# Kernel optimization log

Measured on AMD Instinct MI355X. Metric: run time of the kernel, lower is better.

## Reference

```python
import jax, jax.numpy as jnp
import numpy as np

B, N, H = 8, 128, 512   # batch, num_sent (n == m required by the 'all' branch), hidden_size
D = 2 * H               # bi-LSTM output dim
SCALE = 0.05


def setup_inputs() -> dict:
    key = jax.random.key(0)
    ks = jax.random.split(key, 24)
    p = lambda k, shape: (jax.random.normal(k, shape, dtype=jnp.float32) * SCALE)
    return {
        "x0_enc": jax.random.normal(ks[0], (B, N, D), dtype=jnp.float32),
        "x1_enc": jax.random.normal(ks[1], (B, N, D), dtype=jnp.float32),
        # concat_attention
        "Wc1": p(ks[2], (D, H)), "Wc2": p(ks[3], (D, H)), "vc": p(ks[4], (H,)),
        # bilinear_attention
        "Wb": p(ks[5], (D, D)),
        # dot_attention x2 (separate params)
        "Wd1": p(ks[6], (D, H)), "vd1": p(ks[7], (H,)),
        "Wd2": p(ks[8], (D, H)), "vd2": p(ks[9], (H,)),
        # minus_attention (Ws/vs are unused in forward)
        "Wm": p(ks[10], (D, H)), "vm": p(ks[11], (H,)),
        # aggregation_layer
        "Wq": p(ks[12], (D, H)), "vq": p(ks[13], (H,)),
        "Wp1": p(ks[14], (2 * D, H)), "Wp2": p(ks[15], (D, H)), "vp": p(ks[16], (H,)),
        "Wpred": p(ks[17], (2 * D, 2)), "bpred": jnp.zeros((2,), dtype=jnp.float32),
    }


def _dot_att(x, y, Wd, vd):
    # sjt[b,m,n] = vd . tanh(Wd(x[b,n] * y[b,m]))  -- pairwise elementwise product + MLP
    z = jnp.tanh(jnp.einsum("bnd,bmd,dh->bmnh", x, y, Wd))  # [B,m,n,H]
    s = jnp.einsum("bmnh,h->bmn", z, vd)
    a = jax.nn.softmax(s, axis=2)
    return jnp.einsum("bmn,bnd->bmd", a, x)


def _minus_att(x, y, Wm, vm):
    # Wm is linear, so Wm(x_n - y_m) = (x@Wm)_n - (y@Wm)_m
    a, b = x @ Wm, y @ Wm                                    # [B,n,H], [B,m,H]
    z = jnp.tanh(a[:, None, :, :] - b[:, :, None, :])        # [B,m,n,H]
    s = jnp.einsum("bmnh,h->bmn", z, vm)
    att = jax.nn.softmax(s, axis=2)
    return jnp.einsum("bmn,bnd->bmd", att, x)


def _concat_att(x, y, Wc1, Wc2, vc):
    a, b = x @ Wc1, y @ Wc2                                  # [B,n,H], [B,m,H]
    z = jnp.tanh(a[:, None, :, :] + b[:, :, None, :])        # [B,m,n,H]
    s = jnp.einsum("bmnh,h->bmn", z, vc)
    att = jax.nn.softmax(s, axis=2)
    return jnp.einsum("bmn,bnd->bmd", att, x)


def _bilinear_att(x, y, Wb):
    s = jnp.einsum("bmd,bnd->bmn", y, x @ Wb)
    att = jax.nn.softmax(s, axis=2)
    return jnp.einsum("bmn,bnd->bmd", att, x)


def reference(x0_enc, x1_enc, Wc1, Wc2, vc, Wb, Wd1, vd1, Wd2, vd2, Wm, vm,
              Wq, vq, Wp1, Wp2, vp, Wpred, bpred):
    x0, x1 = x0_enc, x1_enc
    # attention_fx('all')
    qtc = _concat_att(x0, x1, Wc1, Wc2, vc)
    qtb = _bilinear_att(x0, x1, Wb)
    qts = _dot_att(x0, x1, Wd1, vd1)
    qtd = _dot_att(x1, x0, Wd2, vd2)
    qtm = _minus_att(x0, x1, Wm, vm)
    agg_res = jnp.max(jnp.stack([x1, qts, qtc, qtd, qtb, qtm], axis=0), axis=0)  # [B,m,2H]
    # MultiAtt: dropout is identity in eval
    agg_rep = jnp.concatenate([x1, agg_res], axis=2)                             # [B,m,4H]
    # aggregation_layer
    sj = jnp.einsum("bnh,h->bn", jnp.tanh(x0 @ Wq), vq)
    rq = jnp.einsum("bn,bnd->bd", jax.nn.softmax(sj, axis=1), x0)                # [B,2H]
    t = agg_rep @ Wp1 + (rq @ Wp2)[:, None, :]                                   # [B,m,H]
    sp = jax.nn.softmax(jnp.einsum("bmh,h->bm", t, vp), axis=1)
    rp = jnp.einsum("bm,bmd->bd", sp, agg_rep)                                   # [B,4H]
    out = jax.nn.relu(rp @ Wpred + bpred)                                        # [B,2]
    return out
```

## Files before the change

### kernel.cpp

```cpp
#include <hip/hip_runtime.h>
#include <hip/hip_bf16.h>

static constexpr int Bc = 8, Nc = 128, Dc = 1024, Hc = 512;
static constexpr int BM = Bc * Nc;

typedef _Float16 half8 __attribute__((ext_vector_type(8)));
typedef __fp16 fp16x2 __attribute__((ext_vector_type(2)));
typedef float floatx4 __attribute__((ext_vector_type(4)));

__device__ __forceinline__ float fast_tanh(float x) {
  x = fminf(fmaxf(x, -15.f), 15.f);
  float e = __expf(2.f * x);
  return (e - 1.f) / (e + 1.f);
}

__device__ __forceinline__ unsigned pkh2(float a, float b) {
  fp16x2 h = __builtin_amdgcn_cvt_pkrtz(a, b);
  return __builtin_bit_cast(unsigned, h);
}

__device__ __forceinline__ ushort f2h(float f) {
  _Float16 h = (_Float16)f;
  return __builtin_bit_cast(ushort, h);
}

__device__ __forceinline__ float block_sum256(float v, float* buf4) {
  #pragma unroll
  for (int o = 32; o; o >>= 1) v += __shfl_down(v, o, 64);
  const int w = threadIdx.x >> 6, lane = threadIdx.x & 63;
  if (lane == 0) buf4[w] = v;
  __syncthreads();
  return buf4[0] + buf4[1] + buf4[2] + buf4[3];
}

__global__ __launch_bounds__(256) void cvt_both(const float* __restrict__ x0,
                                                const float* __restrict__ x1,
                                                ushort* __restrict__ o0,
                                                ushort* __restrict__ o1) {
  int bi = blockIdx.x;
  const float* src = (bi < 512) ? x0 : x1;
  ushort* dst = (bi < 512) ? o0 : o1;
  int off = (bi & 511);
  int i = (off * 256 + threadIdx.x) * 8;
  float4 a = *reinterpret_cast<const float4*>(&src[i]);
  float4 b = *reinterpret_cast<const float4*>(&src[i + 4]);
  uint4 o;
  o.x = pkh2(a.x, a.y); o.y = pkh2(a.z, a.w);
  o.z = pkh2(b.x, b.y); o.w = pkh2(b.z, b.w);
  *reinterpret_cast<uint4*>(&dst[i]) = o;
}

struct TJobs {
  const float* src[7];
  ushort* dst[7];
  int J[7];
};
__global__ __launch_bounds__(256) void conv_transpose_multi(TJobs jobs) {
  const int job = blockIdx.z;
  const int J = jobs.J[job];
  const int h0 = blockIdx.y * 64;
  if (h0 >= J) return;
  const float* W = jobs.src[job];
  ushort* WT = jobs.dst[job];
  __shared__ float tile[64][65];
  const int d0 = blockIdx.x * 64;
  const int tid = threadIdx.x;
  #pragma unroll
  for (int i = 0; i < 16; i++) {
    int idx = tid + i * 256;
    int dd = idx >> 6, hh = idx & 63;
    tile[dd][hh] = W[(size_t)(d0 + dd) * J + h0 + hh];
  }
  __syncthreads();
  #pragma unroll
  for (int i = 0; i < 16; i++) {
    int idx = tid + i * 256;
    int hh = idx >> 6, dd = idx & 63;
    WT[(size_t)(h0 + hh) * Dc + d0 + dd] = f2h(tile[dd][hh]);
  }
}

__global__ __launch_bounds__(256) void gemm_bt(const ushort* __restrict__ A,
                                               const ushort* __restrict__ BT,
                                               float* __restrict__ Cf,
                                               ushort* __restrict__ Ch,
                                               int K, int ldc,
                                               size_t sA, size_t sB, size_t sC) {
  const int bz = blockIdx.z;
  A  += (size_t)bz * sA;
  BT += (size_t)bz * sB;
  const int m0 = blockIdx.y * 64, n0 = blockIdx.x * 64;
  __shared__ __align__(16) ushort Asl[64][40];
  __shared__ __align__(16) ushort Bsl[64][40];
  const int tid = threadIdx.x, wave = tid >> 6, lane = tid & 63;
  const int quad = lane >> 4, l15 = lane & 15;
  const int wr = (wave & 1) * 32, wc = (wave >> 1) * 32;
  const int rSt = tid >> 2, kSt8 = (tid & 3) * 8;
  floatx4 acc[2][2];
  #pragma unroll
  for (int i = 0; i < 2; i++)
    #pragma unroll
    for (int j = 0; j < 2; j++) acc[i][j] = (floatx4){0.f, 0.f, 0.f, 0.f};
  uint4 pa = *reinterpret_cast<const uint4*>(&A[(size_t)(m0 + rSt) * K + kSt8]);
  uint4 pb = *reinterpret_cast<const uint4*>(&BT[(size_t)(n0 + rSt) * K + kSt8]);
  for (int k0 = 0; k0 < K; k0 += 32) {
    *reinterpret_cast<uint4*>(&Asl[rSt][kSt8]) = pa;
    *reinterpret_cast<uint4*>(&Bsl[rSt][kSt8]) = pb;
    __syncthreads();
    if (k0 + 32 < K) {
      pa = *reinterpret_cast<const uint4*>(&A[(size_t)(m0 + rSt) * K + k0 + 32 + kSt8]);
      pb = *reinterpret_cast<const uint4*>(&BT[(size_t)(n0 + rSt) * K + k0 + 32 + kSt8]);
    }
    half8 af[2], bb[2];
    #pragma unroll
    for (int i = 0; i < 2; i++)
      af[i] = *reinterpret_cast<const half8*>(&Asl[wr + i * 16 + l15][quad * 8]);
    #pragma unroll
    for (int j = 0; j < 2; j++)
      bb[j] = *reinterpret_cast<const half8*>(&Bsl[wc + j * 16 + l15][quad * 8]);
    #pragma unroll
    for (int i = 0; i < 2; i++)
      #pragma unroll
      for (int j = 0; j < 2; j++)
        acc[i][j] = __builtin_amdgcn_mfma_f32_16x16x32_f16(af[i], bb[j], acc[i][j], 0, 0, 0);
    __syncthreads();
  }
  if (Ch) {
    #pragma unroll
    for (int i = 0; i < 2; i++)
      #pragma unroll
      for (int j = 0; j < 2; j++)
        #pragma unroll
        for (int r = 0; r < 4; r++) {
          int row = m0 + wr + i * 16 + quad * 4 + r;
          int col = n0 + wc + j * 16 + l15;
          Ch[(size_t)bz * sC + (size_t)row * ldc + col] = f2h(acc[i][j][r]);
        }
  } else {
    #pragma unroll
    for (int i = 0; i < 2; i++)
      #pragma unroll
      for (int j = 0; j < 2; j++)
        #pragma unroll
        for (int r = 0; r < 4; r++) {
          int row = m0 + wr + i * 16 + quad * 4 + r;
          int col = n0 + wc + j * 16 + l15;
          Cf[(size_t)bz * sC + (size_t)row * ldc + col] = acc[i][j][r];
        }
  }
}

__global__ __launch_bounds__(512, 2) void dot_scores_mfma7(const ushort* __restrict__ X0h,
                                                           const ushort* __restrict__ X1h,
                                                           const ushort* __restrict__ WdT1,
                                                           const ushort* __restrict__ WdT2,
                                                           const float* __restrict__ vd1,
                                                           const float* __restrict__ vd2,
                                                           float* __restrict__ Sd) {
  const int which = blockIdx.z;
  const ushort* Xh = which ? X1h : X0h;
  const ushort* Yh = which ? X0h : X1h;
  const ushort* WdT = which ? WdT2 : WdT1;
  const float* v = which ? vd2 : vd1;
  float* S = Sd + (size_t)which * (BM * Nc);

  const int mp = blockIdx.y;
  const int b = mp >> 6;
  const int hBase = blockIdx.x * 256;
  const int tid = threadIdx.x;
  const int wave = tid >> 6, lane = tid & 63;
  const int quad = lane >> 4, l15 = lane & 15;
  const int mg = wave >> 2, wn = (wave >> 1) & 1, wh = wave & 1;

  __shared__ __align__(16) char smraw[36864];
  ushort* As = (ushort*)smraw;
  ushort* Bs = (ushort*)(smraw + 16384);
  ushort* ylh = (ushort*)(smraw + 32768);
  float (*red)[33] = (float(*)[33])smraw;

  {
    const uint* Y0 = (const uint*)(Yh + (size_t)(mp * 2) * Dc);
    uint* dst = (uint*)ylh;
    dst[tid] = Y0[tid];
    dst[tid + 512] = Y0[tid + 512];
  }

  floatx4 acc[4][8];
  #pragma unroll
  for (int i = 0; i < 4; i++)
    #pragma unroll
    for (int j = 0; j < 8; j++) acc[i][j] = (floatx4){0.f, 0.f, 0.f, 0.f};

  const ushort* Xb = Xh + (size_t)b * Nc * Dc;
  const int nA = tid >> 2;
  const int ch8 = (tid & 3) * 8;

  half8 xv;
  uint4 bv0, bv1;
  auto loads = [&](int s) {
    xv = *reinterpret_cast<const half8*>(Xb + (size_t)nA * Dc + s * 32 + ch8);
    const ushort* wp = WdT + (size_t)(hBase + nA) * Dc + s * 32 + ch8;
    bv0 = *reinterpret_cast<const uint4*>(wp);
    bv1 = *reinterpret_cast<const uint4*>(wp + 128 * Dc);
  };
  auto stage = [&](int s) {
    half8 y0 = *reinterpret_cast<const half8*>(ylh + s * 32 + ch8);
    half8 y1 = *reinterpret_cast<const half8*>(ylh + 1024 + s * 32 + ch8);
    *reinterpret_cast<half8*>(As + (size_t)nA * 32 + ch8) = xv * y0;
    *reinterpret_cast<half8*>(As + 4096 + (size_t)nA * 32 + ch8) = xv * y1;
    *reinterpret_cast<uint4*>(Bs + (size_t)nA * 32 + ch8) = bv0;
    *reinterpret_cast<uint4*>(Bs + 4096 + (size_t)nA * 32 + ch8) = bv1;
  };
  auto mfma_step = [&]() {
    half8 af[4], bfr[8];
    #pragma unroll
    for (int i = 0; i < 4; i++)
      af[i] = *reinterpret_cast<const half8*>(As + mg * 4096 + (wn * 64 + i * 16 + l15) * 32 + quad * 8);
    #pragma unroll
    for (int j = 0; j < 8; j++)
      bfr[j] = *reinterpret_cast<const half8*>(Bs + (wh * 128 + j * 16 + l15) * 32 + quad * 8);
    #pragma unroll
    for (int i = 0; i < 4; i++)
      #pragma unroll
      for (int j = 0; j < 8; j++)
        acc[i][j] = __builtin_amdgcn_mfma_f32_16x16x32_f16(af[i], bfr[j], acc[i][j], 0, 0, 0);
  };

  loads(0);
  __syncthreads();
  #pragma unroll 1
  for (int s = 0; s < 32; s++) {
    stage(s);
    if (s + 1 < 32) loads(s + 1);
    __syncthreads();
    mfma_step();
    __syncthreads();
  }

  float vv[8];
  #pragma unroll
  for (int j = 0; j < 8; j++) vv[j] = v[hBase + wh * 128 + j * 16 + l15];
  #pragma unroll
  for (int i = 0; i < 4; i++)
    #pragma unroll
    for (int r = 0; r < 4; r++) {
      float p = 0.f;
      #pragma unroll
      for (int j = 0; j < 8; j++) p = fmaf(vv[j], fast_tanh(acc[i][j][r]), p);
      red[mg * 128 + wn * 64 + i * 16 + quad * 4 + r][wh * 16 + l15] = p;
    }
  __syncthreads();
  if (tid < 256) {
    float s = 0.f;
    #pragma unroll
    for (int c = 0; c < 32; c++) s += red[tid][c];
    atomicAdd(&S[(size_t)mp * 256 + tid], s);
  }
}

__global__ __launch_bounds__(256) void addtanh_tiled2(const float* __restrict__ C1,
                                                      const float* __restrict__ C2,
                                                      const float* __restrict__ vc,
                                                      const float* __restrict__ vm,
                                                      float* __restrict__ Sc,
                                                      float* __restrict__ Sm) {
  const int nt = blockIdx.x, mt = blockIdx.y;
  const int which = blockIdx.z >> 3, b = blockIdx.z & 7;
  const float* Arow = C1 + which * 512;
  const float* Brow = C2 + which * 512;
  const float* v = which ? vm : vc;
  const float sign = which ? -1.f : 1.f;
  float* S = which ? Sm : Sc;
  __shared__ __align__(16) float at[16][516];
  __shared__ __align__(16) float bt2[16][516];
  __shared__ __align__(16) float vl[512];
  const int tid = threadIdx.x;
  #pragma unroll
  for (int p = 0; p < 8; p++) {
    int idx = p * 256 + tid;
    int r = idx >> 7, c4 = (idx & 127) * 4;
    *reinterpret_cast<float4*>(&at[r][c4]) =
        *reinterpret_cast<const float4*>(&Arow[(size_t)(b * Nc + nt * 16 + r) * 1024 + c4]);
    *reinterpret_cast<float4*>(&bt2[r][c4]) =
        *reinterpret_cast<const float4*>(&Brow[(size_t)(b * Nc + mt * 16 + r) * 1024 + c4]);
  }
  if (tid < 128)
    *reinterpret_cast<float4*>(&vl[tid * 4]) = *reinterpret_cast<const float4*>(&v[tid * 4]);
  __syncthreads();
  const int m = tid >> 4, n = tid & 15;
  float acc = 0.f;
  #pragma unroll 4
  for (int c = 0; c < 512; c += 4) {
    float4 av = *reinterpret_cast<const float4*>(&at[n][c]);
    float4 bv = *reinterpret_cast<const float4*>(&bt2[m][c]);
    float4 vv = *reinterpret_cast<const float4*>(&vl[c]);
    acc = fmaf(vv.x, fast_tanh(fmaf(sign, bv.x, av.x)), acc);
    acc = fmaf(vv.y, fast_tanh(fmaf(sign, bv.y, av.y)), acc);
    acc = fmaf(vv.z, fast_tanh(fmaf(sign, bv.z, av.z)), acc);
    acc = fmaf(vv.w, fast_tanh(fmaf(sign, bv.w, av.w)), acc);
  }
  S[(size_t)(b * Nc + mt * 16 + m) * Nc + nt * 16 + n] = acc;
}

__global__ __launch_bounds__(128) void softmax128(float* __restrict__ S) {
  const int row = blockIdx.x;
  const int tid = threadIdx.x;
  float x = S[(size_t)row * 128 + tid];
  __shared__ float mbuf[2], sbuf[2];
  float mx = x;
  #pragma unroll
  for (int o = 32; o; o >>= 1) mx = fmaxf(mx, __shfl_down(mx, o, 64));
  if ((tid & 63) == 0) mbuf[tid >> 6] = mx;
  __syncthreads();
  mx = fmaxf(mbuf[0], mbuf[1]);
  float e = __expf(x - mx);
  float sm = e;
  #pragma unroll
  for (int o = 32; o; o >>= 1) sm += __shfl_down(sm, o, 64);
  if ((tid & 63) == 0) sbuf[tid >> 6] = sm;
  __syncthreads();
  sm = sbuf[0] + sbuf[1];
  S[(size_t)row * 128 + tid] = e / sm;
}

#define FMA4(acc, s, v)                  \
  acc.x = fmaf(s, v.x, acc.x);           \
  acc.y = fmaf(s, v.y, acc.y);           \
  acc.z = fmaf(s, v.z, acc.z);           \
  acc.w = fmaf(s, v.w, acc.w)

__global__ __launch_bounds__(256) void agg_max(const float* __restrict__ x0,
                                               const float* __restrict__ x1,
                                               const float* __restrict__ Sc,
                                               const float* __restrict__ Sb,
                                               const float* __restrict__ Sd1,
                                               const float* __restrict__ Sd2,
                                               const float* __restrict__ Sm,
                                               const float* __restrict__ u,
                                               float* __restrict__ agg,
                                               float* __restrict__ score) {
  const int bm = blockIdx.x;
  const int b = bm >> 7;
  const int tid = threadIdx.x;
  __shared__ float w[5][128];
  if (tid < 128) {
    w[0][tid] = Sc[(size_t)bm * Nc + tid];
    w[1][tid] = Sb[(size_t)bm * Nc + tid];
    w[2][tid] = Sd1[(size_t)bm * Nc + tid];
    w[3][tid] = Sd2[(size_t)bm * Nc + tid];
    w[4][tid] = Sm[(size_t)bm * Nc + tid];
  }
  __syncthreads();
  const int d0 = tid * 4;
  float4 qc = {0, 0, 0, 0}, qb = {0, 0, 0, 0}, qs = {0, 0, 0, 0};
  float4 qd = {0, 0, 0, 0}, qm = {0, 0, 0, 0};
  const float* X0b = x0 + (size_t)b * Nc * Dc;
  const float* X1b = x1 + (size_t)b * Nc * Dc;
  for (int n = 0; n < Nc; n++) {
    float4 xv = *reinterpret_cast<const float4*>(&X0b[(size_t)n * Dc + d0]);
    float4 yv = *reinterpret_cast<const float4*>(&X1b[(size_t)n * Dc + d0]);
    float wc = w[0][n], wb = w[1][n], ws = w[2][n], wd = w[3][n], wm = w[4][n];
    FMA4(qc, wc, xv);
    FMA4(qb, wb, xv);
    FMA4(qs, ws, xv);
    FMA4(qd, wd, yv);
    FMA4(qm, wm, xv);
  }
  float4 x1v = *reinterpret_cast<const float4*>(&x1[(size_t)bm * Dc + d0]);
  float4 r;
  r.x = fmaxf(x1v.x, fmaxf(fmaxf(qs.x, qc.x), fmaxf(fmaxf(qd.x, qb.x), qm.x)));
  r.y = fmaxf(x1v.y, fmaxf(fmaxf(qs.y, qc.y), fmaxf(fmaxf(qd.y, qb.y), qm.y)));
  r.z = fmaxf(x1v.z, fmaxf(fmaxf(qs.z, qc.z), fmaxf(fmaxf(qd.z, qb.z), qm.z)));
  r.w = fmaxf(x1v.w, fmaxf(fmaxf(qs.w, qc.w), fmaxf(fmaxf(qd.w, qb.w), qm.w)));
  *reinterpret_cast<float4*>(&agg[(size_t)bm * Dc + d0]) = r;
  float4 u1 = *reinterpret_cast<const float4*>(&u[d0]);
  float4 u2 = *reinterpret_cast<const float4*>(&u[Dc + d0]);
  float p = x1v.x * u1.x + x1v.y * u1.y + x1v.z * u1.z + x1v.w * u1.w +
            r.x * u2.x + r.y * u2.y + r.z * u2.z + r.w * u2.w;
  __shared__ float buf4[4];
  p = block_sum256(p, buf4);
  if (tid == 0) score[bm] = p;
}

__global__ __launch_bounds__(64) void compute_u(const float* __restrict__ Wp1,
                                                const float* __restrict__ vp,
                                                float* __restrict__ u) {
  const int d2 = blockIdx.x;
  const int tid = threadIdx.x;
  float p = 0.f;
  #pragma unroll
  for (int h = tid; h < Hc; h += 64) p = fmaf(Wp1[(size_t)d2 * Hc + h], vp[h], p);
  #pragma unroll
  for (int o = 32; o; o >>= 1) p += __shfl_down(p, o, 64);
  if (tid == 0) u[d2] = p;
}

__global__ __launch_bounds__(256) void final_out(const float* __restrict__ x1,
                                                 const float* __restrict__ agg,
                                                 const float* __restrict__ score,
                                                 const float* __restrict__ Wpred,
                                                 const float* __restrict__ bpred,
                                                 float* __restrict__ out) {
  const int b = blockIdx.x;
  const int tid = threadIdx.x;
  __shared__ float spL[128];
  __shared__ float mbuf[2], sbuf[2];
  if (tid < 128) {
    float x = score[b * Nc + tid];
    float mx = x;
    #pragma unroll
    for (int o = 32; o; o >>= 1) mx = fmaxf(mx, __shfl_down(mx, o, 64));
    if ((tid & 63) == 0) mbuf[tid >> 6] = mx;
  }
  __syncthreads();
  if (tid < 128) {
    float x = score[b * Nc + tid];
    float mx = fmaxf(mbuf[0], mbuf[1]);
    float e = __expf(x - mx);
    float sm = e;
    #pragma unroll
    for (int o = 32; o; o >>= 1) sm += __shfl_down(sm, o, 64);
    if ((tid & 63) == 0) sbuf[tid >> 6] = sm;
    spL[tid] = e;
  }
  __syncthreads();
  const float inv = 1.f / (sbuf[0] + sbuf[1]);
  const int d2 = tid * 8;
  float w0[8], w1[8];
  #pragma unroll
  for (int i = 0; i < 8; i++) {
    w0[i] = Wpred[(size_t)(d2 + i) * 2 + 0];
    w1[i] = Wpred[(size_t)(d2 + i) * 2 + 1];
  }
  const float* src = (d2 < Dc) ? (x1 + (size_t)b * Nc * Dc + d2)
                               : (agg + (size_t)b * Nc * Dc + (d2 - Dc));
  float p0 = 0.f, p1 = 0.f;
  for (int m = 0; m < Nc; m++) {
    float s = spL[m] * inv;
    const float* r = src + (size_t)m * Dc;
    #pragma unroll
    for (int i = 0; i < 8; i++) {
      float sc = s * r[i];
      p0 = fmaf(sc, w0[i], p0);
      p1 = fmaf(sc, w1[i], p1);
    }
  }
  #pragma unroll
  for (int o = 32; o; o >>= 1) {
    p0 += __shfl_down(p0, o, 64);
    p1 += __shfl_down(p1, o, 64);
  }
  __shared__ float r0[4], r1[4];
  const int w = tid >> 6, lane = tid & 63;
  if (lane == 0) { r0[w] = p0; r1[w] = p1; }
  __syncthreads();
  if (tid == 0) {
    float q0 = r0[0] + r0[1] + r0[2] + r0[3] + bpred[0];
    float q1 = r1[0] + r1[1] + r1[2] + r1[3] + bpred[1];
    out[b * 2 + 0] = fmaxf(q0, 0.f);
    out[b * 2 + 1] = fmaxf(q1, 0.f);
  }
}

extern "C" void kernel_launch(void* const* d_in, const int* in_sizes, int n_in,
                              void* d_out, int out_size, void* d_ws, size_t ws_size,
                              hipStream_t stream) {
  const float* x0    = (const float*)d_in[0];
  const float* x1    = (const float*)d_in[1];
  const float* Wc1   = (const float*)d_in[2];
  const float* Wc2   = (const float*)d_in[3];
  const float* vc    = (const float*)d_in[4];
  const float* Wb    = (const float*)d_in[5];
  const float* Wd1   = (const float*)d_in[6];
  const float* vd1   = (const float*)d_in[7];
  const float* Wd2   = (const float*)d_in[8];
  const float* vd2   = (const float*)d_in[9];
  const float* Wm    = (const float*)d_in[10];
  const float* vm    = (const float*)d_in[11];
  const float* Wp1   = (const float*)d_in[14];
  const float* vp    = (const float*)d_in[16];
  const float* Wpred = (const float*)d_in[17];
  const float* bpred = (const float*)d_in[18];
  float* out = (float*)d_out;

  float* ws = (float*)d_ws;
  float* C1     = ws;
  float* C2     = C1 + 1048576;
  float* sc     = C2 + 1048576;
  float* sb     = sc + 131072;
  float* sd1    = sb + 131072;
  float* sd2    = sd1 + 131072;
  float* smv    = sd2 + 131072;
  float* u      = smv + 131072;
  float* score2 = u + 2048;
  ushort* x0h   = (ushort*)(score2 + 1024);
  ushort* x1h   = x0h + 1048576;
  ushort* W1T   = x1h + 1048576;
  ushort* W2T   = W1T + 1048576;
  ushort* WbT   = W2T + 1048576;
  ushort* xWbh  = WbT + 1048576;
  ushort* wdT1  = xWbh + 1048576;
  ushort* wdT2  = wdT1 + 524288;
  float* agg    = C1;

  cvt_both<<<1024, 256, 0, stream>>>(x0, x1, x0h, x1h);
  TJobs tj;
  tj.src[0] = Wd1; tj.dst[0] = wdT1;            tj.J[0] = Hc;
  tj.src[1] = Wd2; tj.dst[1] = wdT2;            tj.J[1] = Hc;
  tj.src[2] = Wc1; tj.dst[2] = W1T;             tj.J[2] = Hc;
  tj.src[3] = Wm;  tj.dst[3] = W1T + 512 * Dc;  tj.J[3] = Hc;
  tj.src[4] = Wc2; tj.dst[4] = W2T;             tj.J[4] = Hc;
  tj.src[5] = Wm;  tj.dst[5] = W2T + 512 * Dc;  tj.J[5] = Hc;
  tj.src[6] = Wb;  tj.dst[6] = WbT;             tj.J[6] = Dc;
  conv_transpose_multi<<<dim3(16, 16, 7), 256, 0, stream>>>(tj);
  compute_u<<<2 * Dc, 64, 0, stream>>>(Wp1, vp, u);

  gemm_bt<<<dim3(16, 16, 1), 256, 0, stream>>>(x0h, W1T, C1, nullptr, Dc, 1024, 0, 0, 0);
  gemm_bt<<<dim3(16, 16, 1), 256, 0, stream>>>(x1h, W2T, C2, nullptr, Dc, 1024, 0, 0, 0);
  gemm_bt<<<dim3(16, 16, 1), 256, 0, stream>>>(x0h, WbT, nullptr, xWbh, Dc, 1024, 0, 0, 0);
  gemm_bt<<<dim3(2, 2, 8), 256, 0, stream>>>(x1h, xWbh, sb, nullptr, Dc, 128,
                                             131072, 131072, 16384);

  addtanh_tiled2<<<dim3(8, 8, 16), 256, 0, stream>>>(C1, C2, vc, vm, sc, smv);

  (void)hipMemsetAsync(sd1, 0, 2 * 131072 * sizeof(float), stream);
  dot_scores_mfma7<<<dim3(2, BM / 2, 2), 512, 0, stream>>>(x0h, x1h, wdT1, wdT2, vd1, vd2, sd1);

  softmax128<<<5 * BM, 128, 0, stream>>>(sc);

  agg_max<<<BM, 256, 0, stream>>>(x0, x1, sc, sb, sd1, sd2, smv, u, agg, score2);

  final_out<<<Bc, 256, 0, stream>>>(x1, agg, score2, Wpred, bpred, out);
}
```

Before: 612.5 us.

## Double-buffer LDS in dot-score kernel and apply y-scaling at fragment load

```diff
diff --git a/kernel.cpp b/kernel.cpp
--- a/kernel.cpp
+++ b/kernel.cpp
@@ -150,7 +150,7 @@
   }
 }
 
-__global__ __launch_bounds__(512, 2) void dot_scores_mfma7(const ushort* __restrict__ X0h,
+__global__ __launch_bounds__(512, 2) void dot_scores_mfma8(const ushort* __restrict__ X0h,
                                                            const ushort* __restrict__ X1h,
                                                            const ushort* __restrict__ WdT1,
                                                            const ushort* __restrict__ WdT2,
@@ -172,10 +172,12 @@
   const int quad = lane >> 4, l15 = lane & 15;
   const int mg = wave >> 2, wn = (wave >> 1) & 1, wh = wave & 1;
 
-  __shared__ __align__(16) char smraw[36864];
-  ushort* As = (ushort*)smraw;
-  ushort* Bs = (ushort*)(smraw + 16384);
-  ushort* ylh = (ushort*)(smraw + 32768);
+  __shared__ __align__(16) char smraw[53248];
+  ushort* As0 = (ushort*)smraw;
+  ushort* As1 = (ushort*)(smraw + 8192);
+  ushort* Bs0 = (ushort*)(smraw + 16384);
+  ushort* Bs1 = (ushort*)(smraw + 32768);
+  ushort* ylh = (ushort*)(smraw + 49152);
   float (*red)[33] = (float(*)[33])smraw;
 
   {
@@ -203,22 +205,22 @@
     bv0 = *reinterpret_cast<const uint4*>(wp);
     bv1 = *reinterpret_cast<const uint4*>(wp + 128 * Dc);
   };
-  auto stage = [&](int s) {
-    half8 y0 = *reinterpret_cast<const half8*>(ylh + s * 32 + ch8);
-    half8 y1 = *reinterpret_cast<const half8*>(ylh + 1024 + s * 32 + ch8);
-    *reinterpret_cast<half8*>(As + (size_t)nA * 32 + ch8) = xv * y0;
-    *reinterpret_cast<half8*>(As + 4096 + (size_t)nA * 32 + ch8) = xv * y1;
-    *reinterpret_cast<uint4*>(Bs + (size_t)nA * 32 + ch8) = bv0;
-    *reinterpret_cast<uint4*>(Bs + 4096 + (size_t)nA * 32 + ch8) = bv1;
+  auto stage = [&](ushort* Asb, ushort* Bsb) {
+    *reinterpret_cast<half8*>(Asb + (size_t)nA * 32 + ch8) = xv;
+    *reinterpret_cast<uint4*>(Bsb + (size_t)nA * 32 + ch8) = bv0;
+    *reinterpret_cast<uint4*>(Bsb + 4096 + (size_t)nA * 32 + ch8) = bv1;
   };
-  auto mfma_step = [&]() {
+  auto mfma_step = [&](int s, const ushort* Asb, const ushort* Bsb) {
+    half8 yv = *reinterpret_cast<const half8*>(ylh + mg * 1024 + s * 32 + quad * 8);
     half8 af[4], bfr[8];
     #pragma unroll
-    for (int i = 0; i < 4; i++)
-      af[i] = *reinterpret_cast<const half8*>(As + mg * 4096 + (wn * 64 + i * 16 + l15) * 32 + quad * 8);
+    for (int i = 0; i < 4; i++) {
+      half8 xf = *reinterpret_cast<const half8*>(Asb + (wn * 64 + i * 16 + l15) * 32 + quad * 8);
+      af[i] = xf * yv;
+    }
     #pragma unroll
     for (int j = 0; j < 8; j++)
-      bfr[j] = *reinterpret_cast<const half8*>(Bs + (wh * 128 + j * 16 + l15) * 32 + quad * 8);
+      bfr[j] = *reinterpret_cast<const half8*>(Bsb + (wh * 128 + j * 16 + l15) * 32 + quad * 8);
     #pragma unroll
     for (int i = 0; i < 4; i++)
       #pragma unroll
@@ -227,13 +229,16 @@
   };
 
   loads(0);
+  stage(As0, Bs0);
+  loads(1);
   __syncthreads();
   #pragma unroll 1
   for (int s = 0; s < 32; s++) {
-    stage(s);
-    if (s + 1 < 32) loads(s + 1);
-    __syncthreads();
-    mfma_step();
+    if (s + 1 < 32) {
+      stage((s + 1) & 1 ? As1 : As0, (s + 1) & 1 ? Bs1 : Bs0);
+      if (s + 2 < 32) loads(s + 2);
+    }
+    mfma_step(s, s & 1 ? As1 : As0, s & 1 ? Bs1 : Bs0);
     __syncthreads();
   }
 
@@ -524,7 +529,7 @@
   addtanh_tiled2<<<dim3(8, 8, 16), 256, 0, stream>>>(C1, C2, vc, vm, sc, smv);
 
   (void)hipMemsetAsync(sd1, 0, 2 * 131072 * sizeof(float), stream);
-  dot_scores_mfma7<<<dim3(2, BM / 2, 2), 512, 0, stream>>>(x0h, x1h, wdT1, wdT2, vd1, vd2, sd1);
+  dot_scores_mfma8<<<dim3(2, BM / 2, 2), 512, 0, stream>>>(x0h, x1h, wdT1, wdT2, vd1, vd2, sd1);
 
   softmax128<<<5 * BM, 128, 0, stream>>>(sc);
 
```

After: 624.3 us. No clear change (+1.9%).
